# Performance work log

Measured on AMD Instinct MI355X. Metric: run time of the kernel, lower is better.

The kernel has to match this reference:

```python
import jax, jax.numpy as jnp
import numpy as np

N = 16384      # nodes
E = 262144     # edges (avg degree 16)
R = 9          # relation types
D_IN = 384     # embed_size
D_H = 768      # hidden_size
N_CLASSES = 5


def setup_inputs() -> dict:
    key = jax.random.key(0)
    ks = jax.random.split(key, 11)
    s = 0.02
    return {
        "x": jax.random.normal(ks[0], (N, D_IN), jnp.float32),
        "edge_index": jax.random.randint(ks[1], (2, E), 0, N, dtype=jnp.int64)
        if jax.config.jax_enable_x64 else jax.random.randint(ks[1], (2, E), 0, N).astype(jnp.int32),
        "edge_type": jax.random.randint(ks[2], (E,), 0, R).astype(jnp.int32),
        "rel_W": jax.random.normal(ks[3], (R, D_H, D_IN), jnp.float32) * s,
        "rel_b": jax.random.normal(ks[4], (R, D_H), jnp.float32) * s,
        "norm_constants": jnp.ones((R,), jnp.float32),
        "mp_lin_W": jax.random.normal(ks[5], (D_H, D_H), jnp.float32) * s,
        "mp_lin_b": jax.random.normal(ks[6], (D_H,), jnp.float32) * s,
        "mp_self_W": jax.random.normal(ks[7], (D_H, D_H), jnp.float32) * s,
        "mp_self_b": jax.random.normal(ks[8], (D_H,), jnp.float32) * s,
        "out_W": jax.random.normal(ks[9], (N_CLASSES, D_H), jnp.float32) * s,
        "out_b": jax.random.normal(ks[10], (N_CLASSES,), jnp.float32) * s,
    }


def reference(x, edge_index, edge_type, rel_W, rel_b, norm_constants,
              mp_lin_W, mp_lin_b, mp_self_W, mp_self_b, out_W, out_b):
    n = x.shape[0]
    src = edge_index[0]  # j : message source (x_j)
    dst = edge_index[1]  # i : aggregation target

    # --- RelationAwareMP ---
    # edge_weights[i, j] from x @ x.T, computed per edge (identical math)
    ew = jnp.einsum('ed,ed->e', x[dst], x[src])                  # [E]
    norm = ew / norm_constants[edge_type]                        # [E]
    # per-relation linear applied to all nodes, then gathered per edge
    h = jnp.einsum('nd,rhd->rnh', x, rel_W) + rel_b[:, None, :]  # [R,N,H]
    msg = h[edge_type, src]                                      # [E,H]
    aggr = jax.ops.segment_sum(norm[:, None] * msg, dst, num_segments=n)
    x1 = jax.nn.relu(aggr)                                       # [N,H]

    # --- MP (add aggregation + self transform) ---
    self_x = x1 @ mp_self_W.T + mp_self_b
    hm = x1 @ mp_lin_W.T + mp_lin_b
    aggr2 = jax.ops.segment_sum(hm[src], dst, num_segments=n)
    x2 = jax.nn.relu(aggr2 + self_x)                             # [N,H]

    # --- readout ---
    pooled = x2.mean(axis=0)                                     # [H]
    return pooled @ out_W.T + out_b                              # [N_CLASSES]
```

## Files before the change

### kernel.cpp

```cpp
#include <hip/hip_runtime.h>

typedef unsigned char  u8;
typedef unsigned short u16;
typedef unsigned int   u32;

#define NN   16384
#define EE   262144
#define RR   9
#define DIN  384
#define DH   768
#define KSU  3456
#define KS   3488
#define NPB  4
#define PCOP 16

typedef float  f32x4 __attribute__((ext_vector_type(4)));
typedef float  f32x2 __attribute__((ext_vector_type(2)));
typedef u32    u32x2 __attribute__((ext_vector_type(2)));
typedef __bf16 b16x8 __attribute__((ext_vector_type(8)));

__device__ __forceinline__ u16 f2bf(float f){
  u32 u = __builtin_bit_cast(u32, f);
  u += 0x7fffu + ((u >> 16) & 1u);
  return (u16)(u >> 16);
}
__device__ __forceinline__ float bf2f(u16 h){
  u32 u = ((u32)h) << 16;
  return __builtin_bit_cast(float, u);
}
__device__ __forceinline__ u32 pkbf(float a, float b){
  return (u32)f2bf(a) | ((u32)f2bf(b) << 16);
}
__device__ __forceinline__ void gll16(const void* g, void* l){
  __builtin_amdgcn_global_load_lds((const __attribute__((address_space(1))) void*)g,
                                   (__attribute__((address_space(3))) void*)l, 16, 0, 0);
}
template<int N> __device__ __forceinline__ float dppror(float v){
  return __builtin_bit_cast(float,
    __builtin_amdgcn_update_dpp(0, __builtin_bit_cast(int, v), 0x120+N, 0xF, 0xF, true));
}
__device__ __forceinline__ float swz16(float v){
  return __builtin_bit_cast(float,
    __builtin_amdgcn_ds_swizzle(__builtin_bit_cast(int, v), 0x401F));
}

__global__ void k_count(const int* __restrict__ dst, int* __restrict__ counts){
  const int e = blockIdx.x*256 + threadIdx.x;
  if (e < EE) atomicAdd(&counts[dst[e]], 1);
}

__global__ __launch_bounds__(1024) void k_scan(const int* __restrict__ counts,
                                               int* __restrict__ starts,
                                               int* __restrict__ cursor){
  __shared__ int tot[1024];
  const int t = threadIdx.x;
  int loc[16]; int s = 0;
  #pragma unroll
  for (int j=0;j<16;j++){ loc[j] = counts[t*16+j]; s += loc[j]; }
  tot[t] = s;
  __syncthreads();
  for (int o=1;o<1024;o<<=1){
    int v = (t>=o) ? tot[t-o] : 0;
    __syncthreads();
    tot[t] += v;
    __syncthreads();
  }
  int run = tot[t] - s;
  #pragma unroll
  for (int j=0;j<16;j++){ starts[t*16+j] = run; cursor[t*16+j] = run; run += loc[j]; }
  if (t == 1023) starts[NN] = run;
}

__global__ void k_place(const int* __restrict__ src, const int* __restrict__ dst,
                        const int* __restrict__ et, int* __restrict__ cursor,
                        int* __restrict__ sp){
  const int e = blockIdx.x*256 + threadIdx.x;
  if (e < EE){
    const int p = atomicAdd(&cursor[dst[e]], 1);
    sp[p] = (int)(((u32)et[e] << 28) | (u32)src[e]);
  }
}

__global__ void k_convW1(const float* __restrict__ rW, const float* __restrict__ rb,
                         u16* __restrict__ Wst){
  const int hh = blockIdx.y;
  const int k  = blockIdx.x*256 + threadIdx.x;
  if (k >= KS) return;
  float v;
  if (k < KSU){ const int r = k / DIN; const int d = k - r*DIN;
                v = rW[((long)r*DH + hh)*DIN + d]; }
  else if (k < KSU + RR){ const int r = k - KSU; v = rb[(long)r*DH + hh]; }
  else v = 0.f;
  Wst[(long)hh*KS + k] = f2bf(v);
}

__global__ void k_convW2(const float* __restrict__ lW, const float* __restrict__ sW,
                         u16* __restrict__ WB){
  const int idx = blockIdx.x*256 + threadIdx.x;
  const float v = (idx < DH*DH) ? lW[idx] : sW[idx - DH*DH];
  WB[idx] = f2bf(v);
}

__global__ __launch_bounds__(256, 3) void k_phase1f(const float* __restrict__ x,
                                                    const int* __restrict__ sp,
                                                    const float* __restrict__ nc,
                                                    const int* __restrict__ starts,
                                                    u16* __restrict__ s){
  const int wv = threadIdx.x >> 6;
  const int l  = threadIdx.x & 63;
  const int i  = blockIdx.x*4 + wv;
  const float* xdp = x + (long)i*DIN;
  const f32x4 xq = *(const f32x4*)(xdp + 4*l);
  const f32x2 xr = *(const f32x2*)(xdp + 256 + 2*l);
  float acc[RR][6];
  float cacc[RR];
  #pragma unroll
  for (int r=0;r<RR;r++){
    cacc[r] = 0.f;
    #pragma unroll
    for (int j=0;j<6;j++) acc[r][j] = 0.f;
  }
  const int e0 = starts[i], e1 = starts[i+1];
  f32x4 Aq={0,0,0,0}, Bq={0,0,0,0}, Cq={0,0,0,0}, Dq={0,0,0,0};
  f32x2 Ar={0,0}, Br={0,0}, Cr={0,0}, Dr={0,0};
  u32 qA=0,qB=0,qC=0,qD=0;
  #define LDE(S, QQ, IDX) { const int pe_=(IDX); if (pe_ < e1){ QQ = (u32)sp[pe_]; \
      const float* xs_ = x + (long)(QQ & 0x3FFFu)*DIN; \
      S##q = *(const f32x4*)(xs_ + 4*l); \
      S##r = *(const f32x2*)(xs_ + 256 + 2*l); } }
  LDE(A,qA,e0) LDE(B,qB,e0+1) LDE(C,qC,e0+2) LDE(D,qD,e0+3)
  #define DOT(uq,ur) (xq.x*uq.x + xq.y*uq.y + xq.z*uq.z + xq.w*uq.w \
                    + xr.x*ur.x + xr.y*ur.y)
  #define UPD(R,P,cq,cr) { cacc[R] += P; \
      acc[R][0] += P*cq.x; acc[R][1] += P*cq.y; acc[R][2] += P*cq.z; \
      acc[R][3] += P*cq.w; acc[R][4] += P*cr.x; acc[R][5] += P*cr.y; }
  #define SW(RQ,P,cq,cr) switch (RQ){ \
      case 0: UPD(0,P,cq,cr); break; case 1: UPD(1,P,cq,cr); break; \
      case 2: UPD(2,P,cq,cr); break; case 3: UPD(3,P,cq,cr); break; \
      case 4: UPD(4,P,cq,cr); break; case 5: UPD(5,P,cq,cr); break; \
      case 6: UPD(6,P,cq,cr); break; case 7: UPD(7,P,cq,cr); break; \
      default: UPD(8,P,cq,cr); break; }
  for (int p=e0; p<e1; p+=4){
    const f32x4 aq=Aq, bq=Bq, cq=Cq, dq=Dq;
    const f32x2 ar=Ar, br=Br, cr=Cr, dr=Dr;
    const u32 qa=qA, qb=qB, qc=qC, qd=qD;
    const bool h1 = p+1<e1, h2 = p+2<e1, h3 = p+3<e1;
    LDE(A,qA,p+4) LDE(B,qB,p+5) LDE(C,qC,p+6) LDE(D,qD,p+7)
    float pa = DOT(aq,ar), pb = DOT(bq,br);
    float pc = DOT(cq,cr), pd = DOT(dq,dr);
    pa += dppror<1>(pa); pb += dppror<1>(pb); pc += dppror<1>(pc); pd += dppror<1>(pd);
    pa += dppror<2>(pa); pb += dppror<2>(pb); pc += dppror<2>(pc); pd += dppror<2>(pd);
    pa += dppror<4>(pa); pb += dppror<4>(pb); pc += dppror<4>(pc); pd += dppror<4>(pd);
    pa += dppror<8>(pa); pb += dppror<8>(pb); pc += dppror<8>(pc); pd += dppror<8>(pd);
    pa += swz16(pa); pb += swz16(pb); pc += swz16(pc); pd += swz16(pd);
    pa += __shfl_xor(pa,32); pb += __shfl_xor(pb,32);
    pc += __shfl_xor(pc,32); pd += __shfl_xor(pd,32);
    SW(qa>>28, pa, aq,ar);
    if (h1){ SW(qb>>28, pb, bq,br); }
    if (h2){ SW(qc>>28, pc, cq,cr); }
    if (h3){ SW(qd>>28, pd, dq,dr); }
  }
  #undef LDE
  #undef DOT
  #undef UPD
  #undef SW
  u16* srow = s + (long)i*KS;
  #pragma unroll
  for (int r=0;r<RR;r++){
    const float inv = 1.0f / nc[r];
    const u32 pk0 = pkbf(acc[r][0]*inv, acc[r][1]*inv);
    const u32 pk1 = pkbf(acc[r][2]*inv, acc[r][3]*inv);
    const u32 pk2 = pkbf(acc[r][4]*inv, acc[r][5]*inv);
    *(u32x2*)(srow + r*DIN + 4*l) = (u32x2){pk0, pk1};
    ((u32*)(srow + r*DIN + 256))[l] = pk2;
  }
  float cv = 0.f;
  #pragma unroll
  for (int r=0;r<RR;r++) cv = (l == r) ? cacc[r] : cv;
  if (l < 32){
    const float invl = (l < RR) ? 1.0f/nc[l] : 0.f;
    srow[KSU + l] = f2bf(l < RR ? cv*invl : 0.f);
  }
}

template<int MODE, int NT>
__global__ __launch_bounds__(256, 3)
void k_gemm_bt(const u16* __restrict__ A, const u16* __restrict__ B,
               int K,
               u16* __restrict__ O0, u16* __restrict__ O1,
               const float* __restrict__ b0, const float* __restrict__ b1)
{
  __shared__ __align__(16) u16 As[128*32];
  __shared__ __align__(16) u16 Bs[128*32];
  const int cpx = gridDim.x >> 3;
  const int bid = blockIdx.x;
  const int lg  = (bid & 7)*cpx + (bid >> 3);
  const int mt  = lg / NT;
  const long m0 = (long)mt * 128;
  const long n0 = (long)(lg - mt*NT) * 128;
  const int t  = threadIdx.x;
  const int wv = t >> 6;
  const int ln = t & 63;
  const int wm = wv >> 1, wn = wv & 1;

  const int srow  = ln >> 2;
  const int skcol = (ln & 3) * 8;

  f32x4 acc[4][4];
  #pragma unroll
  for (int i=0;i<4;i++)
    #pragma unroll
    for (int j=0;j<4;j++) acc[i][j] = {0.f,0.f,0.f,0.f};

  const int fr = ln & 15, fq = ln >> 4;
  const int nk = K >> 5;
  for (int kb=0; kb<nk; ++kb){
    const long k0 = (long)kb * 32;
    #pragma unroll
    for (int q=0;q<2;q++){
      const int seg = wv*2 + q;
      const int row = seg*16 + srow;
      gll16(A + (m0 + row)*(long)K + k0 + skcol, &As[seg*512]);
      gll16(B + (n0 + row)*(long)K + k0 + skcol, &Bs[seg*512]);
    }
    __syncthreads();
    b16x8 av[4], bv[4];
    #pragma unroll
    for (int i=0;i<4;i++){
      av[i] = *(const b16x8*)&As[(wm*64 + i*16 + fr)*32 + fq*8];
      bv[i] = *(const b16x8*)&Bs[(wn*64 + i*16 + fr)*32 + fq*8];
    }
    #pragma unroll
    for (int i=0;i<4;i++)
      #pragma unroll
      for (int j=0;j<4;j++)
        acc[i][j] = __builtin_amdgcn_mfma_f32_16x16x32_bf16(av[i], bv[j], acc[i][j], 0, 0, 0);
    __syncthreads();
  }

  #pragma unroll
  for (int i=0;i<4;i++){
    #pragma unroll
    for (int j=0;j<4;j++){
      #pragma unroll
      for (int r=0;r<4;r++){
        const long m = m0 + wm*64 + i*16 + fq*4 + r;
        const long n = n0 + wn*64 + j*16 + fr;
        float v = acc[i][j][r];
        if (MODE == 0){
          v = v > 0.f ? v : 0.f;
          O0[m*DH + n] = f2bf(v);
        } else {
          if (n < DH) O0[m*DH + n]      = f2bf(v + b0[n]);
          else        O1[m*DH + (n-DH)] = f2bf(v + b1[n-DH]);
        }
      }
    }
  }
}

__global__ __launch_bounds__(128) void k_phase2(const u16* __restrict__ hm,
                                                const u16* __restrict__ sfx,
                                                const int* __restrict__ sp,
                                                const int* __restrict__ starts,
                                                float* __restrict__ pooledP){
  const int t  = threadIdx.x;
  const int i0 = blockIdx.x * NPB;
  const int p0 = starts[i0];
  const int pend = starts[i0 + NPB];
  u32 sf00,sf01,sf02, sf10,sf11,sf12, sf20,sf21,sf22, sf30,sf31,sf32;
  { const u32* sr = (const u32*)(sfx + (long)(i0+0)*DH); sf00=sr[t]; sf01=sr[t+128]; sf02=sr[t+256]; }
  { const u32* sr = (const u32*)(sfx + (long)(i0+1)*DH); sf10=sr[t]; sf11=sr[t+128]; sf12=sr[t+256]; }
  { const u32* sr = (const u32*)(sfx + (long)(i0+2)*DH); sf20=sr[t]; sf21=sr[t+128]; sf22=sr[t+256]; }
  { const u32* sr = (const u32*)(sfx + (long)(i0+3)*DH); sf30=sr[t]; sf31=sr[t+128]; sf32=sr[t+256]; }
  u32 A0=0,A1=0,A2=0,B0=0,B1=0,B2=0,C0=0,C1=0,C2=0,D0=0,D1=0,D2=0;
  u32 E0=0,E1=0,E2=0,F0=0,F1=0,F2=0,G0=0,G1=0,G2=0,H0=0,H1=0,H2=0;
  #define PLD(S, IDX) { const int nf_=(IDX); if (nf_ < pend){ \
      const u32* hr_ = (const u32*)(hm + (long)(((u32)sp[nf_]) & 0x3FFFu)*DH); \
      S##0=hr_[t]; S##1=hr_[t+128]; S##2=hr_[t+256]; } }
  PLD(A,p0)   PLD(B,p0+1) PLD(C,p0+2) PLD(D,p0+3)
  PLD(E,p0+4) PLD(F,p0+5) PLD(G,p0+6) PLD(H,p0+7)
  float a0=0.f,a1=0.f,a2=0.f,a3=0.f,a4=0.f,a5=0.f;
  float q0=0.f,q1=0.f,q2=0.f,q3=0.f,q4=0.f,q5=0.f;
  int i = i0;
  int e1 = starts[i0+1];
  #define FLUSH(K) { float v_; \
    v_=a0+bf2f((u16)sf##K##0);        q0+=fmaxf(v_,0.f); \
    v_=a1+bf2f((u16)(sf##K##0>>16));  q1+=fmaxf(v_,0.f); \
    v_=a2+bf2f((u16)sf##K##1);        q2+=fmaxf(v_,0.f); \
    v_=a3+bf2f((u16)(sf##K##1>>16));  q3+=fmaxf(v_,0.f); \
    v_=a4+bf2f((u16)sf##K##2);        q4+=fmaxf(v_,0.f); \
    v_=a5+bf2f((u16)(sf##K##2>>16));  q5+=fmaxf(v_,0.f); \
    a0=a1=a2=a3=a4=a5=0.f; }
  #define FLUSHI { switch (i - i0){ case 0: FLUSH(0); break; case 1: FLUSH(1); break; \
                   case 2: FLUSH(2); break; default: FLUSH(3); break; } }
  while (i < i0+NPB && e1 == p0){ FLUSHI; ++i; e1 = (i < i0+NPB) ? starts[i+1] : 0x7fffffff; }
  #define STEP(S, K) { const int pe_ = base + K; if (pe_ < pend){ \
      const u32 d0_=S##0, d1_=S##1, d2_=S##2; \
      PLD(S, pe_ + 8); \
      a0+=bf2f((u16)d0_); a1+=bf2f((u16)(d0_>>16)); \
      a2+=bf2f((u16)d1_); a3+=bf2f((u16)(d1_>>16)); \
      a4+=bf2f((u16)d2_); a5+=bf2f((u16)(d2_>>16)); \
      while (i < i0+NPB && pe_+1 == e1){ FLUSHI; ++i; \
        e1 = (i < i0+NPB) ? starts[i+1] : 0x7fffffff; } } }
  for (int base = p0; base < pend; base += 8){
    STEP(A,0) STEP(B,1) STEP(C,2) STEP(D,3)
    STEP(E,4) STEP(F,5) STEP(G,6) STEP(H,7)
  }
  while (i < i0+NPB){ FLUSHI; ++i; }
  #undef PLD
  #undef FLUSH
  #undef FLUSHI
  #undef STEP
  float* pd = pooledP + (blockIdx.x & (PCOP-1)) * DH;
  atomicAdd(&pd[2*t],       q0);
  atomicAdd(&pd[2*t+1],     q1);
  atomicAdd(&pd[256+2*t],   q2);
  atomicAdd(&pd[256+2*t+1], q3);
  atomicAdd(&pd[512+2*t],   q4);
  atomicAdd(&pd[512+2*t+1], q5);
}

__global__ __launch_bounds__(256) void k_final(const float* __restrict__ pooledP,
                                               const float* __restrict__ oW,
                                               const float* __restrict__ ob,
                                               float* __restrict__ out){
  __shared__ float ps[DH];
  __shared__ float red[256];
  const int t = threadIdx.x;
  for (int h=t; h<DH; h+=256){
    float s = 0.f;
    #pragma unroll
    for (int c=0;c<PCOP;c++) s += pooledP[c*DH + h];
    ps[h] = s;
  }
  __syncthreads();
  for (int c=0;c<5;c++){
    float p = 0.f;
    for (int h=t; h<DH; h+=256) p += ps[h]*oW[c*DH + h];
    red[t] = p; __syncthreads();
    for (int o=128;o;o>>=1){ if (t<o) red[t]+=red[t+o]; __syncthreads(); }
    if (t == 0) out[c] = red[0]*(1.f/(float)NN) + ob[c];
    __syncthreads();
  }
}

extern "C" void kernel_launch(void* const* d_in, const int* in_sizes, int n_in,
                              void* d_out, int out_size, void* d_ws, size_t ws_size,
                              hipStream_t stream)
{
  (void)in_sizes; (void)n_in; (void)out_size; (void)ws_size;
  const float* x     = (const float*)d_in[0];
  const int*   ei    = (const int*)  d_in[1];
  const int*   et    = (const int*)  d_in[2];
  const float* relW  = (const float*)d_in[3];
  const float* relb  = (const float*)d_in[4];
  const float* nc    = (const float*)d_in[5];
  const float* linW  = (const float*)d_in[6];
  const float* linb  = (const float*)d_in[7];
  const float* selfW = (const float*)d_in[8];
  const float* selfb = (const float*)d_in[9];
  const float* outW  = (const float*)d_in[10];
  const float* outb  = (const float*)d_in[11];
  float* out = (float*)d_out;

  u8* w = (u8*)d_ws;
  int*   counts = (int*)(w + 0);
  int*   starts = (int*)(w + 65536);
  int*   cursor = (int*)(w + 131328);
  int*   srcp   = (int*)(w + 196864);
  u16*   Wst    = (u16*)(w + 4391168);
  u16*   WB     = (u16*)(w + 9748736);
  u16*   x1     = (u16*)(w + 12108032);
  u16*   S      = (u16*)(w + 37276928);
  u16*   hm     = S;
  u16*   sfx    = (u16*)(w + 37276928 + 25165824);
  float* pooledP = (float*)(w + 37276928 + 50331648);

  const int* esrc = ei;
  const int* edst = ei + EE;

  hipMemsetAsync(counts, 0, NN*sizeof(int), stream);

  k_count <<<EE/256, 256, 0, stream>>>(edst, counts);
  k_scan  <<<1, 1024, 0, stream>>>(counts, starts, cursor);
  k_place <<<EE/256, 256, 0, stream>>>(esrc, edst, et, cursor, srcp);
  k_convW1<<<dim3(14, DH), 256, 0, stream>>>(relW, relb, Wst);
  k_convW2<<<(2*DH*DH)/256, 256, 0, stream>>>(linW, selfW, WB);
  k_phase1f<<<NN/4, 256, 0, stream>>>(x, srcp, nc, starts, S);
  k_gemm_bt<0,6><<<(NN/128)*(DH/128), 256, 0, stream>>>(
      S, Wst, KS, x1, (u16*)nullptr, (const float*)nullptr, (const float*)nullptr);
  hipMemsetAsync(pooledP, 0, PCOP*DH*sizeof(float), stream);
  k_gemm_bt<1,12><<<(NN/128)*(2*DH/128), 256, 0, stream>>>(
      x1, WB, DH, hm, sfx, linb, selfb);
  k_phase2<<<NN/NPB, 128, 0, stream>>>(hm, sfx, srcp, starts, pooledP);
  k_final <<<1, 256, 0, stream>>>(pooledP, outW, outb, out);
}
```

Measured before the change: 449.8 us.

## Replace 128x128 GEMM with 256x256 tile, 4-stage LDS pipeline and swizzle

Rewrites the bf16 GEMM to use 256x256 output tiles with 512 threads, each wave computing a 128x64 sub-tile. A 4-deep ring of shared-memory buffers is filled by asynchronous global-to-LDS loads, with explicit vmcnt waits replacing the double __syncthreads per K step. LDS rows are XOR-swizzled to avoid bank conflicts, and s_setprio is raised around the MFMA burst. This is meant to raise data reuse and hide memory latency, at the cost of more LDS (128 KB) and registers per block and fewer blocks in the grid (192 and 384).

```diff
diff --git a/kernel.cpp b/kernel.cpp
--- a/kernel.cpp
+++ b/kernel.cpp
@@ -184,68 +184,84 @@
 }
 
 template<int MODE, int NT>
-__global__ __launch_bounds__(256, 3)
-void k_gemm_bt(const u16* __restrict__ A, const u16* __restrict__ B,
-               int K,
+__global__ __launch_bounds__(512, 2)
+void k_gemm256(const u16* __restrict__ A, const u16* __restrict__ B, int K,
                u16* __restrict__ O0, u16* __restrict__ O1,
                const float* __restrict__ b0, const float* __restrict__ b1)
 {
-  __shared__ __align__(16) u16 As[128*32];
-  __shared__ __align__(16) u16 Bs[128*32];
+  __shared__ __align__(16) u16 lds[4][2][256*32];
   const int cpx = gridDim.x >> 3;
   const int bid = blockIdx.x;
   const int lg  = (bid & 7)*cpx + (bid >> 3);
   const int mt  = lg / NT;
-  const long m0 = (long)mt * 128;
-  const long n0 = (long)(lg - mt*NT) * 128;
-  const int t  = threadIdx.x;
-  const int wv = t >> 6;
-  const int ln = t & 63;
-  const int wm = wv >> 1, wn = wv & 1;
-
-  const int srow  = ln >> 2;
-  const int skcol = (ln & 3) * 8;
-
-  f32x4 acc[4][4];
-  #pragma unroll
-  for (int i=0;i<4;i++)
+  const long m0 = (long)mt * 256;
+  const long n0 = (long)(lg - mt*NT) * 256;
+  const int t   = threadIdx.x;
+  const int wv  = t >> 6;
+  const int ln  = t & 63;
+  const int wm  = wv >> 2;
+  const int wn  = wv & 3;
+  const int fr  = ln & 15, fq = ln >> 4;
+
+  const int lrow  = t >> 2;
+  const int gslot = (t & 3) ^ ((lrow >> 1) & 3);
+
+  f32x4 acc[8][4];
+  #pragma unroll
+  for (int i=0;i<8;i++)
     #pragma unroll
     for (int j=0;j<4;j++) acc[i][j] = {0.f,0.f,0.f,0.f};
 
-  const int fr = ln & 15, fq = ln >> 4;
   const int nk = K >> 5;
-  for (int kb=0; kb<nk; ++kb){
-    const long k0 = (long)kb * 32;
-    #pragma unroll
-    for (int q=0;q<2;q++){
-      const int seg = wv*2 + q;
-      const int row = seg*16 + srow;
-      gll16(A + (m0 + row)*(long)K + k0 + skcol, &As[seg*512]);
-      gll16(B + (n0 + row)*(long)K + k0 + skcol, &Bs[seg*512]);
+
+  #define STAGE(TT) { const int tt_ = (TT); const long k0_ = (long)tt_*32;          \
+    u16* sa_ = &lds[tt_ & 3][0][0]; u16* sb_ = &lds[tt_ & 3][1][0];                 \
+    gll16(A + (m0 +       lrow)*(long)K + k0_ + gslot*8, sa_ + wv*512);             \
+    gll16(A + (m0 + 128 + lrow)*(long)K + k0_ + gslot*8, sa_ + 4096 + wv*512);      \
+    gll16(B + (n0 +       lrow)*(long)K + k0_ + gslot*8, sb_ + wv*512);             \
+    gll16(B + (n0 + 128 + lrow)*(long)K + k0_ + gslot*8, sb_ + 4096 + wv*512); }
+
+  STAGE(0) STAGE(1) STAGE(2)
+  asm volatile("s_waitcnt vmcnt(8)" ::: "memory");
+  __builtin_amdgcn_s_barrier();
+
+  for (int tt = 0; tt < nk; ++tt){
+    if (tt + 3 < nk) STAGE(tt + 3)
+    const u16* sa = &lds[tt & 3][0][0];
+    const u16* sb = &lds[tt & 3][1][0];
+    b16x8 av[8], bv[4];
+    #pragma unroll
+    for (int i=0;i<8;i++){
+      const int row = wm*128 + i*16 + fr;
+      av[i] = *(const b16x8*)((const u8*)sa + row*64 + ((fq ^ ((row>>1)&3)) << 4));
     }
-    __syncthreads();
-    b16x8 av[4], bv[4];
-    #pragma unroll
-    for (int i=0;i<4;i++){
-      av[i] = *(const b16x8*)&As[(wm*64 + i*16 + fr)*32 + fq*8];
-      bv[i] = *(const b16x8*)&Bs[(wn*64 + i*16 + fr)*32 + fq*8];
+    #pragma unroll
+    for (int j=0;j<4;j++){
+      const int row = wn*64 + j*16 + fr;
+      bv[j] = *(const b16x8*)((const u8*)sb + row*64 + ((fq ^ ((row>>1)&3)) << 4));
     }
-    #pragma unroll
-    for (int i=0;i<4;i++)
+    __builtin_amdgcn_s_setprio(1);
+    #pragma unroll
+    for (int i=0;i<8;i++)
       #pragma unroll
       for (int j=0;j<4;j++)
         acc[i][j] = __builtin_amdgcn_mfma_f32_16x16x32_bf16(av[i], bv[j], acc[i][j], 0, 0, 0);
-    __syncthreads();
-  }
-
-  #pragma unroll
-  for (int i=0;i<4;i++){
+    __builtin_amdgcn_s_setprio(0);
+    if (tt + 3 < nk)      asm volatile("s_waitcnt vmcnt(8)" ::: "memory");
+    else if (tt + 2 < nk) asm volatile("s_waitcnt vmcnt(4)" ::: "memory");
+    else if (tt + 1 < nk) asm volatile("s_waitcnt vmcnt(0)" ::: "memory");
+    __builtin_amdgcn_s_barrier();
+  }
+  #undef STAGE
+
+  #pragma unroll
+  for (int i=0;i<8;i++){
     #pragma unroll
     for (int j=0;j<4;j++){
       #pragma unroll
       for (int r=0;r<4;r++){
-        const long m = m0 + wm*64 + i*16 + fq*4 + r;
-        const long n = n0 + wn*64 + j*16 + fr;
+        const long m = m0 + wm*128 + i*16 + fq*4 + r;
+        const long n = n0 + wn*64  + j*16 + fr;
         float v = acc[i][j][r];
         if (MODE == 0){
           v = v > 0.f ? v : 0.f;
@@ -388,10 +404,10 @@
   k_convW1<<<dim3(14, DH), 256, 0, stream>>>(relW, relb, Wst);
   k_convW2<<<(2*DH*DH)/256, 256, 0, stream>>>(linW, selfW, WB);
   k_phase1f<<<NN/4, 256, 0, stream>>>(x, srcp, nc, starts, S);
-  k_gemm_bt<0,6><<<(NN/128)*(DH/128), 256, 0, stream>>>(
+  k_gemm256<0,3><<<(NN/256)*(DH/256), 512, 0, stream>>>(
       S, Wst, KS, x1, (u16*)nullptr, (const float*)nullptr, (const float*)nullptr);
   hipMemsetAsync(pooledP, 0, PCOP*DH*sizeof(float), stream);
-  k_gemm_bt<1,12><<<(NN/128)*(2*DH/128), 256, 0, stream>>>(
+  k_gemm256<1,6><<<(NN/256)*(2*DH/256), 512, 0, stream>>>(
       x1, WB, DH, hm, sfx, linb, selfb);
   k_phase2<<<NN/NPB, 128, 0, stream>>>(hm, sfx, srcp, starts, pooledP);
   k_final <<<1, 256, 0, stream>>>(pooledP, outW, outb, out);
```

Measured after the change: 448.5 us. Within noise of the previous version (-0.3%).

## Triple-buffer GEMM LDS tiles with swizzled layout and MFMA priority boost

Applied to the files above, without the earlier changes.

Replaces the single-buffered GEMM main loop with a three-stage LDS ring. Tiles are prefetched two k-steps ahead via global-to-LDS loads, with one barrier per iteration instead of two. LDS addresses are XOR-swizzled to reduce bank conflicts on the fragment reads, and wave priority is raised around the MFMA block. This aims to hide global load latency in both bf16 GEMMs, at the cost of three times the LDS per block (48KB), which may limit occupancy.

```diff
diff --git a/kernel.cpp b/kernel.cpp
--- a/kernel.cpp
+++ b/kernel.cpp
@@ -185,26 +185,25 @@
 
 template<int MODE, int NT>
 __global__ __launch_bounds__(256, 3)
-void k_gemm_bt(const u16* __restrict__ A, const u16* __restrict__ B,
-               int K,
-               u16* __restrict__ O0, u16* __restrict__ O1,
-               const float* __restrict__ b0, const float* __restrict__ b1)
+void k_gemm128r(const u16* __restrict__ A, const u16* __restrict__ B, int K,
+                u16* __restrict__ O0, u16* __restrict__ O1,
+                const float* __restrict__ b0, const float* __restrict__ b1)
 {
-  __shared__ __align__(16) u16 As[128*32];
-  __shared__ __align__(16) u16 Bs[128*32];
+  __shared__ __align__(16) u16 lds[3][2][128*32];
   const int cpx = gridDim.x >> 3;
   const int bid = blockIdx.x;
   const int lg  = (bid & 7)*cpx + (bid >> 3);
   const int mt  = lg / NT;
   const long m0 = (long)mt * 128;
   const long n0 = (long)(lg - mt*NT) * 128;
-  const int t  = threadIdx.x;
-  const int wv = t >> 6;
-  const int ln = t & 63;
-  const int wm = wv >> 1, wn = wv & 1;
-
-  const int srow  = ln >> 2;
-  const int skcol = (ln & 3) * 8;
+  const int t   = threadIdx.x;
+  const int wv  = t >> 6;
+  const int ln  = t & 63;
+  const int wm  = wv >> 1, wn = wv & 1;
+  const int fr  = ln & 15, fq = ln >> 4;
+
+  const int arow = t >> 2;
+  const int gsl  = (t & 3) ^ ((arow >> 1) & 3);
 
   f32x4 acc[4][4];
   #pragma unroll
@@ -212,31 +211,49 @@
     #pragma unroll
     for (int j=0;j<4;j++) acc[i][j] = {0.f,0.f,0.f,0.f};
 
-  const int fr = ln & 15, fq = ln >> 4;
   const int nk = K >> 5;
-  for (int kb=0; kb<nk; ++kb){
-    const long k0 = (long)kb * 32;
-    #pragma unroll
-    for (int q=0;q<2;q++){
-      const int seg = wv*2 + q;
-      const int row = seg*16 + srow;
-      gll16(A + (m0 + row)*(long)K + k0 + skcol, &As[seg*512]);
-      gll16(B + (n0 + row)*(long)K + k0 + skcol, &Bs[seg*512]);
+
+  #define STAGE(SL, TT) { const long k0_ = (long)(TT)*32;                         \
+    u16* sa_ = &lds[SL][0][0]; u16* sb_ = &lds[SL][1][0];                         \
+    gll16(A + (m0 +      arow)*(long)K + k0_ + gsl*8, sa_ + wv*512);              \
+    gll16(A + (m0 + 64 + arow)*(long)K + k0_ + gsl*8, sa_ + 2048 + wv*512);       \
+    gll16(B + (n0 +      arow)*(long)K + k0_ + gsl*8, sb_ + wv*512);              \
+    gll16(B + (n0 + 64 + arow)*(long)K + k0_ + gsl*8, sb_ + 2048 + wv*512); }
+
+  STAGE(0, 0) STAGE(1, 1)
+  asm volatile("s_waitcnt vmcnt(4)" ::: "memory");
+  __builtin_amdgcn_s_barrier();
+
+  int cs = 0, ps = 2;
+  for (int tt = 0; tt < nk; ++tt){
+    if (tt + 2 < nk) STAGE(ps, tt + 2)
+    const u16* sa = &lds[cs][0][0];
+    const u16* sb = &lds[cs][1][0];
+    b16x8 av[4], bv[4];
+    #pragma unroll
+    for (int i=0;i<4;i++){
+      const int row = wm*64 + i*16 + fr;
+      av[i] = *(const b16x8*)((const u8*)sa + row*64 + ((fq ^ ((row>>1)&3)) << 4));
     }
-    __syncthreads();
-    b16x8 av[4], bv[4];
-    #pragma unroll
-    for (int i=0;i<4;i++){
-      av[i] = *(const b16x8*)&As[(wm*64 + i*16 + fr)*32 + fq*8];
-      bv[i] = *(const b16x8*)&Bs[(wn*64 + i*16 + fr)*32 + fq*8];
+    #pragma unroll
+    for (int j=0;j<4;j++){
+      const int row = wn*64 + j*16 + fr;
+      bv[j] = *(const b16x8*)((const u8*)sb + row*64 + ((fq ^ ((row>>1)&3)) << 4));
     }
+    __builtin_amdgcn_s_setprio(1);
     #pragma unroll
     for (int i=0;i<4;i++)
       #pragma unroll
       for (int j=0;j<4;j++)
         acc[i][j] = __builtin_amdgcn_mfma_f32_16x16x32_bf16(av[i], bv[j], acc[i][j], 0, 0, 0);
-    __syncthreads();
-  }
+    __builtin_amdgcn_s_setprio(0);
+    if (tt + 2 < nk)      asm volatile("s_waitcnt vmcnt(4)" ::: "memory");
+    else if (tt + 1 < nk) asm volatile("s_waitcnt vmcnt(0)" ::: "memory");
+    __builtin_amdgcn_s_barrier();
+    cs = (cs == 2) ? 0 : cs + 1;
+    ps = (ps == 2) ? 0 : ps + 1;
+  }
+  #undef STAGE
 
   #pragma unroll
   for (int i=0;i<4;i++){
@@ -388,10 +405,10 @@
   k_convW1<<<dim3(14, DH), 256, 0, stream>>>(relW, relb, Wst);
   k_convW2<<<(2*DH*DH)/256, 256, 0, stream>>>(linW, selfW, WB);
   k_phase1f<<<NN/4, 256, 0, stream>>>(x, srcp, nc, starts, S);
-  k_gemm_bt<0,6><<<(NN/128)*(DH/128), 256, 0, stream>>>(
+  k_gemm128r<0,6><<<(NN/128)*(DH/128), 256, 0, stream>>>(
       S, Wst, KS, x1, (u16*)nullptr, (const float*)nullptr, (const float*)nullptr);
   hipMemsetAsync(pooledP, 0, PCOP*DH*sizeof(float), stream);
-  k_gemm_bt<1,12><<<(NN/128)*(2*DH/128), 256, 0, stream>>>(
+  k_gemm128r<1,12><<<(NN/128)*(2*DH/128), 256, 0, stream>>>(
       x1, WB, DH, hm, sfx, linb, selfb);
   k_phase2<<<NN/NPB, 128, 0, stream>>>(hm, sfx, srcp, starts, pooledP);
   k_final <<<1, 256, 0, stream>>>(pooledP, outW, outb, out);
```

After: 461.4 us. 1.03x slower.
